# Kernel tuning notes

Hardware: AMD Instinct MI355X
Metric: run time of the kernel (lower is better)

## Reference

```python
import jax, jax.numpy as jnp
import numpy as np

N = 50000      # nodes
E = 800000     # edges (avg degree 16)
F_IN = 128     # in_channels
H = 4          # heads
C = 32         # hidden_channels (per-head out)
L = 3          # num_layers
HC = H * C     # 128 == F_IN so residuals are active


def _layer_norm(x, g, b):
    mu = jnp.mean(x, axis=-1, keepdims=True)
    var = jnp.mean(jnp.square(x - mu), axis=-1, keepdims=True)
    return (x - mu) * jax.lax.rsqrt(var + 1e-5) * g + b


def _gatv2(x, W_l, b_l, W_r, b_r, att, src, dst, concat):
    # GATv2Conv (PyG semantics, eval mode: no dropout)
    xl = (x @ W_l + b_l).reshape(-1, H, C)   # source-side transform  [N,H,C]
    xr = (x @ W_r + b_r).reshape(-1, H, C)   # target-side transform  [N,H,C]
    e = jax.nn.leaky_relu(xl[src] + xr[dst], 0.2)          # [E,H,C]
    alpha = jnp.einsum('ehc,hc->eh', e, att)               # [E,H]
    # segment softmax over incoming edges of each dst node
    m = jax.ops.segment_max(alpha, dst, num_segments=N)    # [N,H]
    a = jnp.exp(alpha - m[dst])
    den = jax.ops.segment_sum(a, dst, num_segments=N) + 1e-16
    a = a / den[dst]
    out = jax.ops.segment_sum(xl[src] * a[:, :, None], dst, num_segments=N)  # [N,H,C]
    if concat:
        return out.reshape(N, HC)
    return out.mean(axis=1)


def setup_inputs() -> dict:
    key = jax.random.key(0)
    ks = jax.random.split(key, 6)
    s = 0.05
    return {
        "x": jax.random.normal(ks[0], (N, F_IN), jnp.float32),
        "edge_index": jax.random.randint(ks[1], (2, E), 0, N, dtype=jnp.int32),
        # all 3 layers have in=128, out=H*C=128 for the linears
        "Wl": jax.random.normal(ks[2], (L, F_IN, HC), jnp.float32) * s,
        "bl": jnp.zeros((L, HC), jnp.float32),
        "Wr": jax.random.normal(ks[3], (L, F_IN, HC), jnp.float32) * s,
        "br": jnp.zeros((L, HC), jnp.float32),
        "att": jax.random.normal(ks[4], (L, H, C), jnp.float32) * s,
        "out_bias01": jnp.zeros((2, HC), jnp.float32),   # concat layers 0,1
        "out_bias2": jnp.zeros((C,), jnp.float32),       # mean layer 2
        "ln_g01": jnp.ones((2, HC), jnp.float32),
        "ln_b01": jnp.zeros((2, HC), jnp.float32),
        "ln_g2": jnp.ones((C,), jnp.float32),
        "ln_b2": jnp.zeros((C,), jnp.float32),
    }


def reference(x, edge_index, Wl, bl, Wr, br, att,
              out_bias01, out_bias2, ln_g01, ln_b01, ln_g2, ln_b2):
    src, dst = edge_index[0], edge_index[1]
    for i in range(L):
        x_in = x
        concat = i < L - 1
        h = _gatv2(x, Wl[i], bl[i], Wr[i], br[i], att[i], src, dst, concat)
        if concat:
            h = h + out_bias01[i]
            h = _layer_norm(h, ln_g01[i], ln_b01[i])
        else:
            h = h + out_bias2
            h = _layer_norm(h, ln_g2, ln_b2)
        h = jax.nn.relu(h)  # dropout omitted (eval mode)
        if i > 0 and h.shape == x_in.shape:
            h = h + x_in
        x = h
    return x
```

## Files before the change

### kernel.cpp

```cpp
#include <hip/hip_runtime.h>
#include <math.h>


#define DPP_QP_XOR1 0xB1
#define DPP_QP_XOR2 0x4E
#define DPP_ROW_MIRROR 0x140
#define DPP_ROW_HALF_MIRROR 0x141

#define EPB 8192
#define MAXB 512
#define ECAP 4096
#define SCAP 4096

template <int CTRL>
__device__ __forceinline__ float dpp_add(float v) {
    int x = __builtin_amdgcn_update_dpp(0, __float_as_int(v), CTRL, 0xf, 0xf, true);
    return v + __int_as_float(x);
}

__device__ __forceinline__ unsigned bf16s(float f) {
    unsigned u = __float_as_uint(f);
    return (u + 0x7fffu + ((u >> 16) & 1u)) >> 16;
}

typedef __bf16 bf16x8 __attribute__((ext_vector_type(8)));
typedef float f32x4 __attribute__((ext_vector_type(4)));
typedef float f32x2 __attribute__((ext_vector_type(2)));


__global__ __launch_bounds__(256) void bin_kernel(
    const int* __restrict__ src, const int* __restrict__ dst,
    int* __restrict__ bucket_count, unsigned* __restrict__ ebuf,
    int E, int NB)
{
    __shared__ int hist[MAXB], lbase[MAXB], gbase[MAXB], cur[MAXB];
    __shared__ int sscan[256];
    __shared__ unsigned stage[EPB];
    const int t = threadIdx.x;
    const int base = blockIdx.x * EPB;
    const int cnt = min(EPB, E - base);

    for (int b = t; b < MAXB; b += 256) hist[b] = 0;
    __syncthreads();
    for (int idx = t; idx < cnt; idx += 256)
        atomicAdd(&hist[dst[base + idx] >> 7], 1);
    __syncthreads();
    {
        const int a = hist[2 * t], b = hist[2 * t + 1];
        sscan[t] = a + b;
        __syncthreads();
        for (int off = 1; off < 256; off <<= 1) {
            int u = (t >= off) ? sscan[t - off] : 0;
            __syncthreads();
            sscan[t] += u;
            __syncthreads();
        }
        const int ex = sscan[t] - (a + b);
        lbase[2 * t] = ex;
        lbase[2 * t + 1] = ex + a;
    }
    __syncthreads();
    for (int b = t; b < NB; b += 256) {
        const int c = hist[b];
        gbase[b] = (c > 0) ? atomicAdd(&bucket_count[b], c) : 0;
        cur[b] = lbase[b];
    }
    __syncthreads();
    for (int idx = t; idx < cnt; idx += 256) {
        const int d = dst[base + idx];
        const int bk = d >> 7;
        const int lp = atomicAdd(&cur[bk], 1);
        stage[lp] = (unsigned)src[base + idx] | ((unsigned)(d & 127) << 16)
                  | ((unsigned)bk << 23);
    }
    __syncthreads();
    for (int idx = t; idx < cnt; idx += 256) {
        const unsigned v = stage[idx];
        const int bk = v >> 23;
        ebuf[(size_t)bk * ECAP + gbase[bk] + (idx - lbase[bk])] = v;
    }
}


__global__ __launch_bounds__(256) void place_kernel(
    const unsigned* __restrict__ ebuf, const int* __restrict__ bucket_count,
    int* __restrict__ row_start, int* __restrict__ deg,
    unsigned short* __restrict__ src_sorted, int Nn, int NB)
{
    __shared__ int hist[128], lexcl[128], cur[128], s[128];
    __shared__ int ptotS;
    __shared__ unsigned short stage[SCAP];
    const int b = blockIdx.x;
    const int t = threadIdx.x;
    const int node0 = b * 128;
    const int cnt = min(bucket_count[b], ECAP);
    const unsigned* eb = ebuf + (size_t)b * ECAP;

    if (t < 128) hist[t] = 0;
    __syncthreads();
    for (int i = t; i < cnt; i += 256)
        atomicAdd(&hist[(eb[i] >> 16) & 127], 1);
    __syncthreads();
    int pv = 0;
    if (t < 128) { pv = (hist[t] + 3) & ~3; s[t] = pv; }
    __syncthreads();
    for (int off = 1; off < 128; off <<= 1) {
        int u = (t >= off && t < 128) ? s[t - off] : 0;
        __syncthreads();
        if (t < 128) s[t] += u;
        __syncthreads();
    }
    if (t < 128) {
        lexcl[t] = s[t] - pv;
        cur[t] = s[t] - pv;
        const int n = node0 + t;
        if (n < Nn) {
            row_start[n] = b * SCAP + lexcl[t];
            deg[n] = hist[t];
        }
    }
    if (t == 127) ptotS = s[127];
    __syncthreads();
    const int ptot = ptotS;
    for (int i = t; i < ptot; i += 256) stage[i] = 0;
    __syncthreads();
    for (int i = t; i < cnt; i += 256) {
        const unsigned v = eb[i];
        const int lp = atomicAdd(&cur[(v >> 16) & 127], 1);
        stage[lp] = (unsigned short)(v & 0xffffu);
    }
    __syncthreads();
    for (int i = t; i < ptot; i += 256)
        src_sorted[(size_t)b * SCAP + i] = stage[i];
}


__global__ __launch_bounds__(256) void prep_kernel(
    const float* __restrict__ x, const float* __restrict__ Wl,
    const float* __restrict__ Wr, unsigned* __restrict__ xb,
    unsigned short* __restrict__ Bt, int n8, int btTotal)
{
    const int idx = blockIdx.x * blockDim.x + threadIdx.x;
    if (idx < n8) {
        const float4 a = reinterpret_cast<const float4*>(x)[idx * 2];
        const float4 b = reinterpret_cast<const float4*>(x)[idx * 2 + 1];
        uint4 o;
        o.x = bf16s(a.x) | (bf16s(a.y) << 16);
        o.y = bf16s(a.z) | (bf16s(a.w) << 16);
        o.z = bf16s(b.x) | (bf16s(b.y) << 16);
        o.w = bf16s(b.z) | (bf16s(b.w) << 16);
        reinterpret_cast<uint4*>(xb)[idx] = o;
    }
    if (idx < btTotal) {
        const int k = idx & 127;
        const int n = (idx >> 7) & 255;
        const int l = idx >> 15;
        const float v = (n < 128) ? Wl[l * 16384 + k * 128 + n]
                                  : Wr[l * 16384 + k * 128 + (n - 128)];
        Bt[idx] = (unsigned short)bf16s(v);
    }
}


__global__ __launch_bounds__(256) void gemm_mfma(
    const unsigned short* __restrict__ Xb, const unsigned short* __restrict__ Bt,
    const float* __restrict__ bl, const float* __restrict__ br,
    unsigned short* __restrict__ XLb, unsigned short* __restrict__ XRb, int Nn)
{
    const int t = threadIdx.x;
    const int lane = t & 63;
    const int w = t >> 6;
    const int n0 = w * 64;
    const int l15 = lane & 15;
    const int kg = lane >> 4;
    const int rowBase = blockIdx.x * 32;

    f32x4 acc[2][4] = {};

    int ra[2];
    ra[0] = min(rowBase + l15, Nn - 1);
    ra[1] = min(rowBase + 16 + l15, Nn - 1);

#pragma unroll
    for (int ks = 0; ks < 4; ++ks) {
        const int k0 = ks * 32 + kg * 8;
        bf16x8 a[2];
        a[0] = *reinterpret_cast<const bf16x8*>(Xb + (size_t)ra[0] * 128 + k0);
        a[1] = *reinterpret_cast<const bf16x8*>(Xb + (size_t)ra[1] * 128 + k0);
#pragma unroll
        for (int nt = 0; nt < 4; ++nt) {
            const int col = n0 + nt * 16 + l15;
            const bf16x8 b = *reinterpret_cast<const bf16x8*>(Bt + (size_t)col * 128 + k0);
            acc[0][nt] = __builtin_amdgcn_mfma_f32_16x16x32_bf16(a[0], b, acc[0][nt], 0, 0, 0);
            acc[1][nt] = __builtin_amdgcn_mfma_f32_16x16x32_bf16(a[1], b, acc[1][nt], 0, 0, 0);
        }
    }

    const bool isXL = (w < 2);
#pragma unroll
    for (int mt = 0; mt < 2; ++mt) {
#pragma unroll
        for (int nt = 0; nt < 4; ++nt) {
            const int col = n0 + nt * 16 + l15;
            const float bv = isXL ? bl[col] : br[col - 128];
#pragma unroll
            for (int r = 0; r < 4; ++r) {
                const int row = rowBase + mt * 16 + kg * 4 + r;
                if (row >= Nn) continue;
                const float v = acc[mt][nt][r] + bv;
                if (isXL) XLb[(size_t)row * 128 + col] = (unsigned short)bf16s(v);
                else      XRb[(size_t)row * 128 + (col - 128)] = (unsigned short)bf16s(v);
            }
        }
    }
}


__device__ __forceinline__ void unpack8(const uint4 q, f32x2* v) {
    v[0] = f32x2{__uint_as_float(q.x << 16), __uint_as_float(q.x & 0xffff0000u)};
    v[1] = f32x2{__uint_as_float(q.y << 16), __uint_as_float(q.y & 0xffff0000u)};
    v[2] = f32x2{__uint_as_float(q.z << 16), __uint_as_float(q.z & 0xffff0000u)};
    v[3] = f32x2{__uint_as_float(q.w << 16), __uint_as_float(q.w & 0xffff0000u)};
}

__device__ __forceinline__ void edge_accum(const uint4 q, const f32x2* xr, const f32x2* av,
                                           const bool dead, float& wsum, f32x2* acc) {
    f32x2 xl[4];
    unpack8(q, xl);
    f32x2 pd = {0.f, 0.f};
#pragma unroll
    for (int j = 0; j < 4; ++j) {
        f32x2 tt = xl[j] + xr[j];
        tt = __builtin_elementwise_max(tt, tt * 0.2f);
        pd += tt * av[j];
    }
    float part = pd.x + pd.y;
    part = dpp_add<DPP_QP_XOR1>(part);
    part = dpp_add<DPP_QP_XOR2>(part);
    if (dead) part = -INFINITY;
    const float e = __expf(part);
    wsum += e;
    const f32x2 e2 = {e, e};
#pragma unroll
    for (int j = 0; j < 4; ++j) acc[j] += e2 * xl[j];
}

template <int MODE>
__global__ __launch_bounds__(256) void aggregate_kernel(
    const unsigned* __restrict__ XLb, const unsigned* __restrict__ XRb,
    const int* __restrict__ row_start, const int* __restrict__ deg,
    const unsigned short* __restrict__ src_sorted,
    const float* __restrict__ att, const float* __restrict__ obias,
    const float* __restrict__ lng, const float* __restrict__ lnb,
    const unsigned* __restrict__ residb, float* __restrict__ out,
    unsigned* __restrict__ outb, int Nn)
{
    const int lane = threadIdx.x & 63;
    const int wid = threadIdx.x >> 6;
    const int node = blockIdx.x * 4 + wid;
    if (node >= Nn) return;
    const int g = lane >> 4;
    const int i = lane & 15;
    const int c0 = i * 8;

    f32x2 xr[4], av[4];
    {
        const uint4 qr = reinterpret_cast<const uint4*>(XRb)[(size_t)node * 16 + i];
        unpack8(qr, xr);
        const float4 c = *reinterpret_cast<const float4*>(att + c0);
        const float4 d = *reinterpret_cast<const float4*>(att + c0 + 4);
        av[0] = f32x2{c.x, c.y}; av[1] = f32x2{c.z, c.w};
        av[2] = f32x2{d.x, d.y}; av[3] = f32x2{d.z, d.w};
    }

    f32x2 acc[4] = {};
    float wsum = 0.f;

    const int p0 = row_start[node];
    const int dg = deg[node];
    const int p1 = p0 + dg;

    if (dg > 0) {
        int sA = src_sorted[p0 + g];
        int sB = src_sorted[p0 + 4 + g];
        for (int p = p0; p < p1; p += 8) {
            const int sAn = src_sorted[p + 8 + g];
            const int sBn = src_sorted[p + 12 + g];
            const uint4 qA = reinterpret_cast<const uint4*>(XLb)[(size_t)sA * 16 + i];
            edge_accum(qA, xr, av, p + g >= p1, wsum, acc);
            if (p + 4 < p1) {
                const uint4 qB = reinterpret_cast<const uint4*>(XLb)[(size_t)sB * 16 + i];
                edge_accum(qB, xr, av, p + 4 + g >= p1, wsum, acc);
            }
            sA = sAn;
            sB = sBn;
        }
    }

    wsum += __shfl_xor(wsum, 16); wsum += __shfl_xor(wsum, 32);
    float o[8];
#pragma unroll
    for (int j = 0; j < 4; ++j) { o[2 * j] = acc[j].x; o[2 * j + 1] = acc[j].y; }
#pragma unroll
    for (int j = 0; j < 8; ++j) {
        o[j] += __shfl_xor(o[j], 16);
        o[j] += __shfl_xor(o[j], 32);
    }

    const float inv = 1.f / (wsum + 1e-16f);
#pragma unroll
    for (int j = 0; j < 8; ++j) o[j] *= inv;

    if (MODE < 2) {
        float v[8], d[8];
        float s = 0.f;
#pragma unroll
        for (int j = 0; j < 8; ++j) { v[j] = o[j] + obias[c0 + j]; s += v[j]; }
        s = dpp_add<DPP_QP_XOR1>(s); s = dpp_add<DPP_QP_XOR2>(s);
        s = dpp_add<DPP_ROW_MIRROR>(s); s = dpp_add<DPP_ROW_HALF_MIRROR>(s);
        const float mu = s * (1.f / 128.f);
        float q = 0.f;
#pragma unroll
        for (int j = 0; j < 8; ++j) { d[j] = v[j] - mu; q = fmaf(d[j], d[j], q); }
        q = dpp_add<DPP_QP_XOR1>(q); q = dpp_add<DPP_QP_XOR2>(q);
        q = dpp_add<DPP_ROW_MIRROR>(q); q = dpp_add<DPP_ROW_HALF_MIRROR>(q);
        const float rstd = rsqrtf(q * (1.f / 128.f) + 1e-5f);
        float h[8];
#pragma unroll
        for (int j = 0; j < 8; ++j)
            h[j] = fmaxf(d[j] * rstd * lng[c0 + j] + lnb[c0 + j], 0.f);
        if (MODE == 1) {
            const uint4 qr2 = reinterpret_cast<const uint4*>(residb)[(size_t)node * 16 + i];
            f32x2 rr[4];
            unpack8(qr2, rr);
            h[0] += rr[0].x; h[1] += rr[0].y; h[2] += rr[1].x; h[3] += rr[1].y;
            h[4] += rr[2].x; h[5] += rr[2].y; h[6] += rr[3].x; h[7] += rr[3].y;
        }
        if (g == 0) {
            uint4 pb;
            pb.x = bf16s(h[0]) | (bf16s(h[1]) << 16);
            pb.y = bf16s(h[2]) | (bf16s(h[3]) << 16);
            pb.z = bf16s(h[4]) | (bf16s(h[5]) << 16);
            pb.w = bf16s(h[6]) | (bf16s(h[7]) << 16);
            reinterpret_cast<uint4*>(outb)[(size_t)node * 16 + i] = pb;
        }
    } else {
#pragma unroll
        for (int j = 0; j < 8; ++j) {
            o[j] += __shfl_xor(o[j], 4);
            o[j] += __shfl_xor(o[j], 8);
            o[j] *= 0.25f;
        }
        const int cb = (i & 3) * 8;
        float v[8], d[8];
        float s = 0.f;
#pragma unroll
        for (int j = 0; j < 8; ++j) { v[j] = o[j] + obias[cb + j]; s += v[j]; }
        s = dpp_add<DPP_QP_XOR1>(s); s = dpp_add<DPP_QP_XOR2>(s);
        const float mu = s * (1.f / 32.f);
        float q = 0.f;
#pragma unroll
        for (int j = 0; j < 8; ++j) { d[j] = v[j] - mu; q = fmaf(d[j], d[j], q); }
        q = dpp_add<DPP_QP_XOR1>(q); q = dpp_add<DPP_QP_XOR2>(q);
        const float rstd = rsqrtf(q * (1.f / 32.f) + 1e-5f);
        float h[8];
#pragma unroll
        for (int j = 0; j < 8; ++j)
            h[j] = fmaxf(d[j] * rstd * lng[cb + j] + lnb[cb + j], 0.f);
        if (lane < 4) {
            *reinterpret_cast<float4*>(out + (size_t)node * 32 + cb) =
                make_float4(h[0], h[1], h[2], h[3]);
            *reinterpret_cast<float4*>(out + (size_t)node * 32 + cb + 4) =
                make_float4(h[4], h[5], h[6], h[7]);
        }
    }
}

extern "C" void kernel_launch(void* const* d_in, const int* in_sizes, int n_in,
                              void* d_out, int out_size, void* d_ws, size_t ws_size,
                              hipStream_t stream)
{
    const float* x    = (const float*)d_in[0];
    const int*   ei   = (const int*)d_in[1];
    const float* Wl   = (const float*)d_in[2];
    const float* bl   = (const float*)d_in[3];
    const float* Wr   = (const float*)d_in[4];
    const float* br   = (const float*)d_in[5];
    const float* att  = (const float*)d_in[6];
    const float* ob01 = (const float*)d_in[7];
    const float* ob2  = (const float*)d_in[8];
    const float* lg01 = (const float*)d_in[9];
    const float* lb01 = (const float*)d_in[10];
    const float* lg2  = (const float*)d_in[11];
    const float* lb2  = (const float*)d_in[12];
    float* outp = (float*)d_out;

    const int Nn = in_sizes[0] / 128;
    const int E  = in_sizes[1] / 2;
    const int* srcI = ei;
    const int* dstI = ei + E;
    const int NB = (Nn + 127) / 128;

    char* ws = (char*)d_ws;
    size_t off = 0;
    auto alloc = [&](size_t bytes) {
        void* p = ws + off;
        off += (bytes + 255) & ~(size_t)255;
        return p;
    };
    unsigned short* Xb0   = (unsigned short*)alloc((size_t)Nn * 128 * 2);
    unsigned short* XLb   = (unsigned short*)alloc((size_t)Nn * 128 * 2);
    unsigned short* XRb   = (unsigned short*)alloc((size_t)Nn * 128 * 2);
    unsigned short* bufAb = (unsigned short*)alloc((size_t)Nn * 128 * 2);
    unsigned short* bufBb = (unsigned short*)alloc((size_t)Nn * 128 * 2);
    unsigned short* Bt    = (unsigned short*)alloc((size_t)3 * 256 * 128 * 2);
    int*   row_start      = (int*)alloc((size_t)Nn * 4);
    int*   deg            = (int*)alloc((size_t)Nn * 4);
    unsigned short* src_sorted = (unsigned short*)alloc((size_t)NB * SCAP * 2 + 256);
    unsigned* ebuf        = (unsigned*)alloc((size_t)NB * ECAP * 4);
    int*   bucket_cnt     = (int*)alloc((size_t)MAXB * 4);
    (void)ws_size;

    const int btTotal = 3 * 256 * 128;

    hipMemsetAsync(bucket_cnt, 0, (size_t)NB * 4, stream);
    prep_kernel<<<(Nn * 16 + 255) / 256, 256, 0, stream>>>(x, Wl, Wr, (unsigned*)Xb0, Bt,
                                                           Nn * 16, btTotal);
    bin_kernel<<<(E + EPB - 1) / EPB, 256, 0, stream>>>(srcI, dstI, bucket_cnt, ebuf, E, NB);
    place_kernel<<<NB, 256, 0, stream>>>(ebuf, bucket_cnt, row_start, deg, src_sorted, Nn, NB);

    const int gemm_grid = (Nn + 31) / 32;
    const int agg_grid  = (Nn + 3) / 4;

    gemm_mfma<<<gemm_grid, 256, 0, stream>>>(Xb0, Bt, bl, br, XLb, XRb, Nn);
    aggregate_kernel<0><<<agg_grid, 256, 0, stream>>>((const unsigned*)XLb, (const unsigned*)XRb,
        row_start, deg, src_sorted, att, ob01, lg01, lb01, nullptr, nullptr,
        (unsigned*)bufAb, Nn);

    gemm_mfma<<<gemm_grid, 256, 0, stream>>>(bufAb, Bt + 32768, bl + 128, br + 128, XLb, XRb, Nn);
    aggregate_kernel<1><<<agg_grid, 256, 0, stream>>>((const unsigned*)XLb, (const unsigned*)XRb,
        row_start, deg, src_sorted, att + 128, ob01 + 128, lg01 + 128, lb01 + 128,
        (const unsigned*)bufAb, nullptr, (unsigned*)bufBb, Nn);

    gemm_mfma<<<gemm_grid, 256, 0, stream>>>(bufBb, Bt + 65536, bl + 256, br + 256, XLb, XRb, Nn);
    aggregate_kernel<2><<<agg_grid, 256, 0, stream>>>((const unsigned*)XLb, (const unsigned*)XRb,
        row_start, deg, src_sorted, att + 256, ob2, lg2, lb2, nullptr, outp, nullptr, Nn);
}
```

Before: 260.6 us.

## Fuse x bf16 conversion into first GEMM, zero bucket counts in prep, widen gather loop

```diff
diff --git a/kernel.cpp b/kernel.cpp
--- a/kernel.cpp
+++ b/kernel.cpp
@@ -136,21 +136,11 @@
 
 
 __global__ __launch_bounds__(256) void prep_kernel(
-    const float* __restrict__ x, const float* __restrict__ Wl,
-    const float* __restrict__ Wr, unsigned* __restrict__ xb,
-    unsigned short* __restrict__ Bt, int n8, int btTotal)
+    const float* __restrict__ Wl, const float* __restrict__ Wr,
+    unsigned short* __restrict__ Bt, int* __restrict__ bucket_cnt, int btTotal)
 {
     const int idx = blockIdx.x * blockDim.x + threadIdx.x;
-    if (idx < n8) {
-        const float4 a = reinterpret_cast<const float4*>(x)[idx * 2];
-        const float4 b = reinterpret_cast<const float4*>(x)[idx * 2 + 1];
-        uint4 o;
-        o.x = bf16s(a.x) | (bf16s(a.y) << 16);
-        o.y = bf16s(a.z) | (bf16s(a.w) << 16);
-        o.z = bf16s(b.x) | (bf16s(b.y) << 16);
-        o.w = bf16s(b.z) | (bf16s(b.w) << 16);
-        reinterpret_cast<uint4*>(xb)[idx] = o;
-    }
+    if (idx < MAXB) bucket_cnt[idx] = 0;
     if (idx < btTotal) {
         const int k = idx & 127;
         const int n = (idx >> 7) & 255;
@@ -162,8 +152,9 @@
 }
 
 
+template <bool F32A>
 __global__ __launch_bounds__(256) void gemm_mfma(
-    const unsigned short* __restrict__ Xb, const unsigned short* __restrict__ Bt,
+    const void* __restrict__ Xv, const unsigned short* __restrict__ Bt,
     const float* __restrict__ bl, const float* __restrict__ br,
     unsigned short* __restrict__ XLb, unsigned short* __restrict__ XRb, int Nn)
 {
@@ -185,8 +176,23 @@
     for (int ks = 0; ks < 4; ++ks) {
         const int k0 = ks * 32 + kg * 8;
         bf16x8 a[2];
-        a[0] = *reinterpret_cast<const bf16x8*>(Xb + (size_t)ra[0] * 128 + k0);
-        a[1] = *reinterpret_cast<const bf16x8*>(Xb + (size_t)ra[1] * 128 + k0);
+#pragma unroll
+        for (int mt = 0; mt < 2; ++mt) {
+            if constexpr (F32A) {
+                const float* X = (const float*)Xv;
+                const float4 f0 = *reinterpret_cast<const float4*>(X + (size_t)ra[mt] * 128 + k0);
+                const float4 f1 = *reinterpret_cast<const float4*>(X + (size_t)ra[mt] * 128 + k0 + 4);
+                bf16x8 av;
+                av[0] = (__bf16)f0.x; av[1] = (__bf16)f0.y;
+                av[2] = (__bf16)f0.z; av[3] = (__bf16)f0.w;
+                av[4] = (__bf16)f1.x; av[5] = (__bf16)f1.y;
+                av[6] = (__bf16)f1.z; av[7] = (__bf16)f1.w;
+                a[mt] = av;
+            } else {
+                const unsigned short* Xb = (const unsigned short*)Xv;
+                a[mt] = *reinterpret_cast<const bf16x8*>(Xb + (size_t)ra[mt] * 128 + k0);
+            }
+        }
 #pragma unroll
         for (int nt = 0; nt < 4; ++nt) {
             const int col = n0 + nt * 16 + l15;
@@ -277,24 +283,22 @@
     float wsum = 0.f;
 
     const int p0 = row_start[node];
-    const int dg = deg[node];
-    const int p1 = p0 + dg;
-
-    if (dg > 0) {
-        int sA = src_sorted[p0 + g];
-        int sB = src_sorted[p0 + 4 + g];
-        for (int p = p0; p < p1; p += 8) {
-            const int sAn = src_sorted[p + 8 + g];
-            const int sBn = src_sorted[p + 12 + g];
-            const uint4 qA = reinterpret_cast<const uint4*>(XLb)[(size_t)sA * 16 + i];
-            edge_accum(qA, xr, av, p + g >= p1, wsum, acc);
-            if (p + 4 < p1) {
-                const uint4 qB = reinterpret_cast<const uint4*>(XLb)[(size_t)sB * 16 + i];
-                edge_accum(qB, xr, av, p + 4 + g >= p1, wsum, acc);
-            }
-            sA = sAn;
-            sB = sBn;
-        }
+    const int p1 = p0 + deg[node];
+    const uint4* XL4 = reinterpret_cast<const uint4*>(XLb);
+
+    for (int p = p0; p < p1; p += 16) {
+        const int s0 = src_sorted[p + g];
+        const int s1 = src_sorted[p + 4 + g];
+        const int s2 = src_sorted[p + 8 + g];
+        const int s3 = src_sorted[p + 12 + g];
+        const uint4 q0 = XL4[(size_t)s0 * 16 + i];
+        const uint4 q1 = XL4[(size_t)s1 * 16 + i];
+        const uint4 q2 = XL4[(size_t)s2 * 16 + i];
+        const uint4 q3 = XL4[(size_t)s3 * 16 + i];
+        edge_accum(q0, xr, av, p + g >= p1, wsum, acc);
+        if (p + 4 < p1)  edge_accum(q1, xr, av, p + 4 + g >= p1, wsum, acc);
+        if (p + 8 < p1)  edge_accum(q2, xr, av, p + 8 + g >= p1, wsum, acc);
+        if (p + 12 < p1) edge_accum(q3, xr, av, p + 12 + g >= p1, wsum, acc);
     }
 
     wsum += __shfl_xor(wsum, 16); wsum += __shfl_xor(wsum, 32);
@@ -408,7 +412,6 @@
         off += (bytes + 255) & ~(size_t)255;
         return p;
     };
-    unsigned short* Xb0   = (unsigned short*)alloc((size_t)Nn * 128 * 2);
     unsigned short* XLb   = (unsigned short*)alloc((size_t)Nn * 128 * 2);
     unsigned short* XRb   = (unsigned short*)alloc((size_t)Nn * 128 * 2);
     unsigned short* bufAb = (unsigned short*)alloc((size_t)Nn * 128 * 2);
@@ -423,26 +426,26 @@
 
     const int btTotal = 3 * 256 * 128;
 
-    hipMemsetAsync(bucket_cnt, 0, (size_t)NB * 4, stream);
-    prep_kernel<<<(Nn * 16 + 255) / 256, 256, 0, stream>>>(x, Wl, Wr, (unsigned*)Xb0, Bt,
-                                                           Nn * 16, btTotal);
+    prep_kernel<<<(btTotal + 255) / 256, 256, 0, stream>>>(Wl, Wr, Bt, bucket_cnt, btTotal);
     bin_kernel<<<(E + EPB - 1) / EPB, 256, 0, stream>>>(srcI, dstI, bucket_cnt, ebuf, E, NB);
     place_kernel<<<NB, 256, 0, stream>>>(ebuf, bucket_cnt, row_start, deg, src_sorted, Nn, NB);
 
     const int gemm_grid = (Nn + 31) / 32;
     const int agg_grid  = (Nn + 3) / 4;
 
-    gemm_mfma<<<gemm_grid, 256, 0, stream>>>(Xb0, Bt, bl, br, XLb, XRb, Nn);
+    gemm_mfma<true><<<gemm_grid, 256, 0, stream>>>(x, Bt, bl, br, XLb, XRb, Nn);
     aggregate_kernel<0><<<agg_grid, 256, 0, stream>>>((const unsigned*)XLb, (const unsigned*)XRb,
         row_start, deg, src_sorted, att, ob01, lg01, lb01, nullptr, nullptr,
         (unsigned*)bufAb, Nn);
 
-    gemm_mfma<<<gemm_grid, 256, 0, stream>>>(bufAb, Bt + 32768, bl + 128, br + 128, XLb, XRb, Nn);
+    gemm_mfma<false><<<gemm_grid, 256, 0, stream>>>(bufAb, Bt + 32768, bl + 128, br + 128,
+                                                    XLb, XRb, Nn);
     aggregate_kernel<1><<<agg_grid, 256, 0, stream>>>((const unsigned*)XLb, (const unsigned*)XRb,
         row_start, deg, src_sorted, att + 128, ob01 + 128, lg01 + 128, lb01 + 128,
         (const unsigned*)bufAb, nullptr, (unsigned*)bufBb, Nn);
 
-    gemm_mfma<<<gemm_grid, 256, 0, stream>>>(bufBb, Bt + 65536, bl + 256, br + 256, XLb, XRb, Nn);
+    gemm_mfma<false><<<gemm_grid, 256, 0, stream>>>(bufBb, Bt + 65536, bl + 256, br + 256,
+                                                    XLb, XRb, Nn);
     aggregate_kernel<2><<<agg_grid, 256, 0, stream>>>((const unsigned*)XLb, (const unsigned*)XRb,
         row_start, deg, src_sorted, att + 256, ob2, lg2, lb2, nullptr, outp, nullptr, Nn);
 }
```

New measurement: 271.5 us. 4.2% more time.
